# Kernel tuning notes

Hardware: AMD Instinct MI355X
Metric: run time of the kernel (lower is better)

## Reference

```python
import jax, jax.numpy as jnp
import numpy as np

B, L, T, LM, DFF, D, H = 8, 256, 2048, 4096, 1024, 84, 4
HD = D // H  # 21
NCLS = 265


def _ln(x, s, b):
    m = x.mean(-1, keepdims=True)
    v = ((x - m) ** 2).mean(-1, keepdims=True)
    return (x - m) * jax.lax.rsqrt(v + 1e-5) * s + b


def _fourier(xyz, gB):
    # PositionEmbeddingCoordsSine(d_pos=10, pos_type='fourier'): xyz @ B * 2pi -> [sin, cos]
    proj = (2.0 * jnp.pi) * jnp.einsum('bnc,cd->bnd', xyz, gB)  # [B,N,5]
    return jnp.concatenate([jnp.sin(proj), jnp.cos(proj)], axis=-1)  # [B,N,10]


def setup_inputs() -> dict:
    key = jax.random.key(0)
    ks = jax.random.split(key, 20)
    def nrm(k, shape, scale):
        return jax.random.normal(k, shape, jnp.float32) * scale
    coords = jax.random.uniform(ks[0], (B, L, 6), jnp.float32)
    cls = jax.random.randint(ks[1], (B, L), 0, NCLS).astype(jnp.float32)
    vision_features = jnp.concatenate([coords, cls[..., None]], axis=-1)  # [B,L,7]
    FIN = D * L + LM  # 25600
    inp = {
        'grd_tokens': nrm(ks[2], (T, LM), 1.0),
        'vision_features': vision_features,
        'token_batch_idx': jax.random.randint(ks[3], (T,), 0, B),
        'gauss_B': nrm(ks[4], (3, 5), 1.0),
        'class_emb': nrm(ks[5], (NCLS, 64), 0.02),
        'w_in': nrm(ks[6], (2, D, 3 * D), D ** -0.5),
        'b_in': jnp.zeros((2, 3 * D), jnp.float32),
        'w_out': nrm(ks[7], (2, D, D), D ** -0.5),
        'b_out': jnp.zeros((2, D), jnp.float32),
        'ln1_s': jnp.ones((2, D), jnp.float32), 'ln1_b': jnp.zeros((2, D), jnp.float32),
        'w_ff1': nrm(ks[8], (2, D, DFF), D ** -0.5), 'b_ff1': jnp.zeros((2, DFF), jnp.float32),
        'w_ff2': nrm(ks[9], (2, DFF, D), DFF ** -0.5), 'b_ff2': jnp.zeros((2, D), jnp.float32),
        'ln2_s': jnp.ones((2, D), jnp.float32), 'ln2_b': jnp.zeros((2, D), jnp.float32),
        'w0': nrm(ks[10], (FIN, DFF), FIN ** -0.5), 'b0': jnp.zeros((DFF,), jnp.float32),
        'w1': nrm(ks[11], (DFF, DFF), DFF ** -0.5), 'b1': jnp.zeros((DFF,), jnp.float32),
        'w2': nrm(ks[12], (DFF, DFF), DFF ** -0.5), 'b2': jnp.zeros((DFF,), jnp.float32),
        'w3': nrm(ks[13], (DFF, DFF), DFF ** -0.5), 'b3': jnp.zeros((DFF,), jnp.float32),
        'w4': nrm(ks[14], (DFF, 6), DFF ** -0.5), 'b4': jnp.zeros((6,), jnp.float32),
    }
    return inp


def reference(grd_tokens, vision_features, token_batch_idx, gauss_B, class_emb,
              w_in, b_in, w_out, b_out, ln1_s, ln1_b, w_ff1, b_ff1, w_ff2, b_ff2,
              ln2_s, ln2_b, w0, b0, w1, b1, w2, b2, w3, b3, w4, b4):
    pe_min = _fourier(vision_features[:, :, 0:3], gauss_B)  # [B,L,10]
    pe_max = _fourier(vision_features[:, :, 3:6], gauss_B)  # [B,L,10]
    cls = vision_features[:, :, -1].astype(jnp.int32)
    src = jnp.concatenate([pe_min, pe_max, class_emb[cls]], axis=-1)  # [B,L,84]
    pad = jnp.all(vision_features == 0, axis=-1)  # [B,L]
    neg = jnp.where(pad, -1e9, 0.0)[:, None, None, :]  # [B,1,1,L] key-padding bias
    # 2-layer post-norm transformer encoder (DETR-style, pos=None, dropout=0)
    for l in range(2):
        qkv = src @ w_in[l] + b_in[l]
        q, k, v = jnp.split(qkv, 3, axis=-1)
        q = q.reshape(B, L, H, HD)
        k = k.reshape(B, L, H, HD)
        v = v.reshape(B, L, H, HD)
        scores = jnp.einsum('blhd,bmhd->bhlm', q, k) / jnp.sqrt(jnp.float32(HD)) + neg
        attn = jax.nn.softmax(scores, axis=-1)
        o = jnp.einsum('bhlm,bmhd->blhd', attn, v).reshape(B, L, D)
        src = _ln(src + o @ w_out[l] + b_out[l], ln1_s[l], ln1_b[l])
        ff = jax.nn.relu(src @ w_ff1[l] + b_ff1[l]) @ w_ff2[l] + b_ff2[l]
        src = _ln(src + ff, ln2_s[l], ln2_b[l])
    vision_flat = src.reshape(B, L * D)  # flattened encoder output per sample [B, 21504]
    # batched version of the ragged python loop: gather per-token vision feat + concat lm feat
    feat = jnp.concatenate([vision_flat[token_batch_idx], grd_tokens], axis=-1)  # [T, 25600]
    h = jax.nn.relu(feat @ w0 + b0)
    h = jax.nn.relu(h @ w1 + b1)
    h = jax.nn.relu(h @ w2 + b2)
    h = jax.nn.relu(h @ w3 + b3)
    return h @ w4 + b4  # [T, 6]
```

## Files before the change

kernel.cpp:

```cpp
#include <hip/hip_runtime.h>
#include <hip/hip_bf16.h>

#define B_ 8
#define L_ 256
#define T_ 2048
#define LM_ 4096
#define DFF_ 1024
#define D_ 84
#define H_ 4
#define HD_ 21
#define BL_ (B_*L_)
#define VISF_ (L_*D_)
#define VKS 168
#define VCHUNK (VISF_/VKS)
#define AKS 8
#define AKEYS (L_/AKS)

typedef __attribute__((ext_vector_type(8))) short bf16x8;
typedef __attribute__((ext_vector_type(4))) float f32x4;

typedef const __attribute__((address_space(1))) int* gas_p;
typedef __attribute__((address_space(3))) int* las_p;
__device__ __forceinline__ void gld_lds16(const void* g, void* l) {
    __builtin_amdgcn_global_load_lds((gas_p)g, (las_p)l, 16, 0, 0);
}

__global__ void k_build_src(const float* __restrict__ vf, const float* __restrict__ gB,
                            const float* __restrict__ cemb, float* __restrict__ src,
                            float* __restrict__ neg)
{
    int row = blockIdx.x * blockDim.x + threadIdx.x;
    if (row >= BL_) return;
    float v[7];
    bool allz = true;
    #pragma unroll
    for (int c = 0; c < 7; ++c) { v[c] = vf[row*7 + c]; allz = allz && (v[c] == 0.0f); }
    neg[row] = allz ? -1e9f : 0.0f;
    float* s = src + (size_t)row * D_;
    const float TWO_PI = 6.28318530717958647692f;
    #pragma unroll
    for (int d = 0; d < 5; ++d) {
        float pmin = TWO_PI * (v[0]*gB[d] + v[1]*gB[5+d] + v[2]*gB[10+d]);
        float pmax = TWO_PI * (v[3]*gB[d] + v[4]*gB[5+d] + v[5]*gB[10+d]);
        s[d]      = sinf(pmin);  s[5+d]  = cosf(pmin);
        s[10+d]   = sinf(pmax);  s[15+d] = cosf(pmax);
    }
    int cls = (int)v[6];
    const float4* ce = reinterpret_cast<const float4*>(cemb + (size_t)cls*64);
    float4* so = reinterpret_cast<float4*>(s + 20);
    #pragma unroll
    for (int i = 0; i < 16; ++i) so[i] = ce[i];
}

__global__ __launch_bounds__(256) void k_qkv8(const float* __restrict__ src,
        const float* __restrict__ w_in, const float* __restrict__ b_in,
        float* __restrict__ qkv, int lay)
{
    __shared__ float s8[8][D_];
    int r0 = blockIdx.x * 8, tid = threadIdx.x;
    for (int idx = tid; idx < 8*D_; idx += 256) {
        int r = idx / D_, d = idx - r*D_;
        s8[r][d] = src[(size_t)(r0+r)*D_ + d];
    }
    __syncthreads();
    if (tid < 3*D_) {
        const float* w = w_in + (size_t)lay*D_*3*D_ + tid;
        float acc[8] = {};
        for (int d = 0; d < D_; ++d) {
            float wv = w[(size_t)d*3*D_];
            #pragma unroll
            for (int r = 0; r < 8; ++r) acc[r] = fmaf(s8[r][d], wv, acc[r]);
        }
        float bv = b_in[lay*3*D_ + tid];
        #pragma unroll
        for (int r = 0; r < 8; ++r) qkv[(size_t)(r0+r)*(3*D_) + tid] = acc[r] + bv;
    }
}

__global__ __launch_bounds__(256) void k_attn_part(const float* __restrict__ qkv,
        const float* __restrict__ neg, float* __restrict__ part)
{
    __shared__ float ks_[AKEYS*HD_], vs_[AKEYS*HD_], ns[AKEYS];
    int bh = blockIdx.x;
    int b = bh >> 2, h = bh & 3;
    int sp = blockIdx.y;
    int tid = threadIdx.x;
    int k0 = sp * AKEYS;
    for (int idx = tid; idx < AKEYS*HD_; idx += 256) {
        int l = idx / HD_, d = idx - l*HD_;
        size_t base = ((size_t)(b*L_ + k0 + l))*(3*D_) + h*HD_ + d;
        ks_[idx] = qkv[base + D_];
        vs_[idx] = qkv[base + 2*D_];
    }
    if (tid < AKEYS) ns[tid] = neg[b*L_ + k0 + tid];
    __syncthreads();
    float q[HD_];
    {
        size_t base = ((size_t)(b*L_ + tid))*(3*D_) + h*HD_;
        #pragma unroll
        for (int d = 0; d < HD_; ++d) q[d] = qkv[base + d];
    }
    const float scale = 0.21821789023599239f;
    float m_run = -INFINITY, l_run = 0.0f;
    float o[HD_];
    #pragma unroll
    for (int d = 0; d < HD_; ++d) o[d] = 0.0f;
    for (int m = 0; m < AKEYS; ++m) {
        const float* krow = &ks_[m*HD_];
        float sdot = 0.0f;
        #pragma unroll
        for (int d = 0; d < HD_; ++d) sdot = fmaf(q[d], krow[d], sdot);
        float sc = sdot * scale + ns[m];
        float nm = fmaxf(m_run, sc);
        float c = __expf(m_run - nm);
        float p = __expf(sc - nm);
        l_run = l_run * c + p;
        const float* vrow = &vs_[m*HD_];
        #pragma unroll
        for (int d = 0; d < HD_; ++d) o[d] = fmaf(p, vrow[d], o[d]*c);
        m_run = nm;
    }
    float* po = part + (((size_t)bh*AKS + sp)*L_ + tid)*24;
    #pragma unroll
    for (int d = 0; d < HD_; ++d) po[d] = o[d];
    po[21] = m_run;
    po[22] = l_run;
}

__global__ __launch_bounds__(64) void k_attn_merge(const float* __restrict__ part,
        float* __restrict__ attn_o)
{
    int bh = blockIdx.x;
    int b = bh >> 2, h = bh & 3;
    int q = blockIdx.y*64 + threadIdx.x;
    const float* pb = part + ((size_t)bh*AKS*L_ + q)*24;
    float m_tot = -INFINITY;
    #pragma unroll
    for (int sp = 0; sp < AKS; ++sp)
        m_tot = fmaxf(m_tot, pb[(size_t)sp*L_*24 + 21]);
    float l_tot = 0.0f;
    float o[HD_];
    #pragma unroll
    for (int d = 0; d < HD_; ++d) o[d] = 0.0f;
    #pragma unroll
    for (int sp = 0; sp < AKS; ++sp) {
        const float* pp = pb + (size_t)sp*L_*24;
        float e = __expf(pp[21] - m_tot);
        l_tot = fmaf(pp[22], e, l_tot);
        #pragma unroll
        for (int d = 0; d < HD_; ++d) o[d] = fmaf(pp[d], e, o[d]);
    }
    float inv = 1.0f / l_tot;
    float* op = attn_o + ((size_t)(b*L_ + q))*D_ + h*HD_;
    #pragma unroll
    for (int d = 0; d < HD_; ++d) op[d] = o[d]*inv;
}

__global__ __launch_bounds__(128) void k_oproj_ln(const float* __restrict__ attn_o,
        const float* __restrict__ w_out, const float* __restrict__ b_out,
        const float* __restrict__ ln_s, const float* __restrict__ ln_b,
        float* __restrict__ src, __hip_bfloat16* __restrict__ srcb, int lay)
{
    __shared__ float os[D_];
    __shared__ float r1[128], r2[128];
    int row = blockIdx.x, tid = threadIdx.x;
    if (tid < D_) os[tid] = attn_o[(size_t)row*D_ + tid];
    __syncthreads();
    float y = 0.0f;
    if (tid < D_) {
        const float* w = w_out + (size_t)lay*D_*D_ + tid;
        float acc = b_out[lay*D_ + tid];
        for (int d = 0; d < D_; ++d) acc = fmaf(os[d], w[(size_t)d*D_], acc);
        y = src[(size_t)row*D_ + tid] + acc;
    }
    r1[tid] = (tid < D_) ? y : 0.0f;
    r2[tid] = (tid < D_) ? y*y : 0.0f;
    __syncthreads();
    for (int s = 64; s > 0; s >>= 1) {
        if (tid < s) { r1[tid] += r1[tid+s]; r2[tid] += r2[tid+s]; }
        __syncthreads();
    }
    float mean = r1[0] * (1.0f/D_);
    float var  = r2[0] * (1.0f/D_) - mean*mean;
    float rstd = rsqrtf(var + 1e-5f);
    float out = 0.0f;
    if (tid < D_) {
        out = (y - mean)*rstd*ln_s[lay*D_+tid] + ln_b[lay*D_+tid];
        src[(size_t)row*D_ + tid] = out;
    }
    srcb[(size_t)row*128 + tid] = (tid < D_) ? __float2bfloat16(out)
                                             : __float2bfloat16(0.0f);
}

__global__ __launch_bounds__(256) void k_ff2_mfma(
        const __hip_bfloat16* __restrict__ hb,
        const __hip_bfloat16* __restrict__ wt,
        float* __restrict__ part)
{
    __shared__ __align__(16) __hip_bfloat16 sA[2][4096];
    __shared__ __align__(16) __hip_bfloat16 sB[2][6144];
    int tid = threadIdx.x;
    int bm = blockIdx.x * 64, sp = blockIdx.y;
    int wave = tid >> 6, lane = tid & 63;
    int wr = wave >> 1, wc = wave & 1;
    int l15 = lane & 15, l4 = lane >> 4;
    f32x4 acc[2][3] = {};

    const int a_m0 = tid & 63;
    const int b_i0 = tid,       b_kb0 = b_i0/96, b_n0 = b_i0%96;
    const int b_i1 = tid + 256, b_kb1 = b_i1/96, b_n1 = b_i1%96;
    const int b_i2 = tid + 512, b_kb2 = b_i2/96, b_n2 = b_i2%96;
    const __hip_bfloat16* Ap0 = hb + (size_t)(bm + a_m0)*1024 + sp*128 + (tid>>6)*8;
    const __hip_bfloat16* Ap1 = Ap0 + 32;
    const __hip_bfloat16* Bp0 = wt + (size_t)b_n0*1024 + sp*128 + b_kb0*8;
    const __hip_bfloat16* Bp1 = wt + (size_t)b_n1*1024 + sp*128 + b_kb1*8;
    const __hip_bfloat16* Bp2 = wt + (size_t)b_n2*1024 + sp*128 + b_kb2*8;

    gld_lds16(Ap0, (char*)&sA[0][0] + tid*16);
    gld_lds16(Ap1, (char*)&sA[0][0] + (tid+256)*16);
    gld_lds16(Bp0, (char*)&sB[0][0] + b_i0*16);
    gld_lds16(Bp1, (char*)&sB[0][0] + b_i1*16);
    gld_lds16(Bp2, (char*)&sB[0][0] + b_i2*16);
    #pragma unroll
    for (int t = 0; t < 2; ++t) {
        __syncthreads();
        if (t == 0) {
            gld_lds16(Ap0 + 64, (char*)&sA[1][0] + tid*16);
            gld_lds16(Ap1 + 64, (char*)&sA[1][0] + (tid+256)*16);
            gld_lds16(Bp0 + 64, (char*)&sB[1][0] + b_i0*16);
            gld_lds16(Bp1 + 64, (char*)&sB[1][0] + b_i1*16);
            gld_lds16(Bp2 + 64, (char*)&sB[1][0] + b_i2*16);
        }
        const __hip_bfloat16* sa = &sA[t][0];
        const __hip_bfloat16* sb = &sB[t][0];
        #pragma unroll
        for (int ks = 0; ks < 2; ++ks) {
            bf16x8 af[2], bfr[3];
            #pragma unroll
            for (int mi = 0; mi < 2; ++mi)
                af[mi] = *reinterpret_cast<const bf16x8*>(
                    &sa[(size_t)((ks*4 + l4)*64 + wr*32 + mi*16 + l15) * 8]);
            #pragma unroll
            for (int ni = 0; ni < 3; ++ni)
                bfr[ni] = *reinterpret_cast<const bf16x8*>(
                    &sb[(size_t)((ks*4 + l4)*96 + wc*48 + ni*16 + l15) * 8]);
            #pragma unroll
            for (int mi = 0; mi < 2; ++mi)
                #pragma unroll
                for (int ni = 0; ni < 3; ++ni)
                    acc[mi][ni] = __builtin_amdgcn_mfma_f32_16x16x32_bf16(
                        af[mi], bfr[ni], acc[mi][ni], 0, 0, 0);
        }
    }
    float* po = part + (size_t)sp*(2048*96);
    #pragma unroll
    for (int mi = 0; mi < 2; ++mi)
        #pragma unroll
        for (int reg = 0; reg < 4; ++reg) {
            int row = bm + wr*32 + mi*16 + l4*4 + reg;
            #pragma unroll
            for (int ni = 0; ni < 3; ++ni) {
                int col = wc*48 + ni*16 + l15;
                po[(size_t)row*96 + col] = acc[mi][ni][reg];
            }
        }
}

__global__ __launch_bounds__(128) void k_ff2ln_red(const float* __restrict__ part,
        const float* __restrict__ b_ff2, const float* __restrict__ ln_s,
        const float* __restrict__ ln_b, float* __restrict__ src, int lay)
{
    __shared__ float r1[128], r2[128];
    int row = blockIdx.x, tid = threadIdx.x;
    float y = 0.0f;
    if (tid < D_) {
        #pragma unroll
        for (int sp = 0; sp < 8; ++sp)
            y += part[(size_t)sp*(2048*96) + (size_t)row*96 + tid];
        y += b_ff2[lay*D_ + tid] + src[(size_t)row*D_ + tid];
    }
    r1[tid] = (tid < D_) ? y : 0.0f;
    r2[tid] = (tid < D_) ? y*y : 0.0f;
    __syncthreads();
    for (int s = 64; s > 0; s >>= 1) {
        if (tid < s) { r1[tid] += r1[tid+s]; r2[tid] += r2[tid+s]; }
        __syncthreads();
    }
    float mean = r1[0] * (1.0f/D_);
    float var  = r2[0] * (1.0f/D_) - mean*mean;
    float rstd = rsqrtf(var + 1e-5f);
    if (tid < D_)
        src[(size_t)row*D_ + tid] = (y - mean)*rstd*ln_s[lay*D_+tid] + ln_b[lay*D_+tid];
}

__global__ __launch_bounds__(256) void k_vis_gemm(const float* __restrict__ src,
        const float* __restrict__ w0, float* __restrict__ partials)
{
    __shared__ float vf[8][VCHUNK];
    __shared__ float red[8][256][4];
    int nt = blockIdx.x, sp = blockIdx.y, tid = threadIdx.x;
    int k0 = sp * VCHUNK;
    for (int idx = tid; idx < 8*VCHUNK; idx += 256) {
        int r = idx >> 7, c = idx & 127;
        vf[r][c] = src[(size_t)r*VISF_ + k0 + c];
    }
    __syncthreads();
    int ng = tid & 31;
    int kh = tid >> 5;
    const float* wp = w0 + (size_t)(k0 + kh*16)*DFF_ + nt*128 + ng*4;
    float acc[8][4] = {};
    #pragma unroll 4
    for (int kk = 0; kk < 16; ++kk) {
        float4 w = *reinterpret_cast<const float4*>(wp + (size_t)kk*DFF_);
        #pragma unroll
        for (int m = 0; m < 8; ++m) {
            float sv = vf[m][kh*16 + kk];
            acc[m][0] = fmaf(sv, w.x, acc[m][0]);
            acc[m][1] = fmaf(sv, w.y, acc[m][1]);
            acc[m][2] = fmaf(sv, w.z, acc[m][2]);
            acc[m][3] = fmaf(sv, w.w, acc[m][3]);
        }
    }
    #pragma unroll
    for (int m = 0; m < 8; ++m)
        *reinterpret_cast<float4*>(&red[m][tid][0]) =
            make_float4(acc[m][0], acc[m][1], acc[m][2], acc[m][3]);
    __syncthreads();
    int m2 = tid >> 5, ng2 = tid & 31;
    float4 s = *reinterpret_cast<const float4*>(&red[m2][ng2][0]);
    #pragma unroll
    for (int j = 1; j < 8; ++j) {
        float4 v = *reinterpret_cast<const float4*>(&red[m2][j*32 + ng2][0]);
        s.x += v.x; s.y += v.y; s.z += v.z; s.w += v.w;
    }
    *reinterpret_cast<float4*>(
        &partials[(size_t)sp*8192 + m2*1024 + nt*128 + ng2*4]) = s;
}

__global__ __launch_bounds__(256) void k_vis_red1(const float* __restrict__ partials,
        float* __restrict__ p2)
{
    int o = blockIdx.x*256 + threadIdx.x;
    int g = blockIdx.y;
    float s = 0.0f;
    #pragma unroll
    for (int j = 0; j < 14; ++j) s += partials[(size_t)(g*14 + j)*8192 + o];
    p2[(size_t)g*8192 + o] = s;
}

__global__ __launch_bounds__(256) void k_vis_red2(const float* __restrict__ p2,
        float* __restrict__ vis)
{
    int o = blockIdx.x*256 + threadIdx.x;
    float s = 0.0f;
    #pragma unroll
    for (int g = 0; g < 12; ++g) s += p2[(size_t)g*8192 + o];
    vis[o] = s;
}

struct bh4 { __hip_bfloat16 x, y, z, w; };

__global__ __launch_bounds__(256) void k_f2b(const float* __restrict__ in,
        __hip_bfloat16* __restrict__ out, int n4)
{
    int i = blockIdx.x*256 + threadIdx.x;
    if (i >= n4) return;
    float4 v = reinterpret_cast<const float4*>(in)[i];
    bh4 o = { __float2bfloat16(v.x), __float2bfloat16(v.y),
              __float2bfloat16(v.z), __float2bfloat16(v.w) };
    reinterpret_cast<bh4*>(out)[i] = o;
}

__global__ __launch_bounds__(256) void k_wT(const float* __restrict__ W,
        __hip_bfloat16* __restrict__ WT, int K, int N)
{
    __shared__ float t[32][33];
    int kb = blockIdx.x*32, nb = blockIdx.y*32;
    int tx = threadIdx.x & 31, ty = threadIdx.x >> 5;
    #pragma unroll
    for (int i = 0; i < 4; ++i)
        t[ty + i*8][tx] = W[(size_t)(kb + ty + i*8)*N + nb + tx];
    __syncthreads();
    #pragma unroll
    for (int i = 0; i < 4; ++i)
        WT[(size_t)(nb + ty + i*8)*K + kb + tx] = __float2bfloat16(t[tx][ty + i*8]);
}

__global__ __launch_bounds__(256) void k_wTp(const float* __restrict__ W,
        __hip_bfloat16* __restrict__ WT, int K, int N, int KP)
{
    __shared__ float t[32][33];
    int kb = blockIdx.x*32, nb = blockIdx.y*32;
    int tx = threadIdx.x & 31, ty = threadIdx.x >> 5;
    #pragma unroll
    for (int i = 0; i < 4; ++i) {
        int k = kb + ty + i*8, n = nb + tx;
        t[ty + i*8][tx] = (k < K && n < N) ? W[(size_t)k*N + n] : 0.0f;
    }
    __syncthreads();
    #pragma unroll
    for (int i = 0; i < 4; ++i)
        WT[(size_t)(nb + ty + i*8)*KP + kb + tx] = __float2bfloat16(t[tx][ty + i*8]);
}

template<bool ADD_VIS>
__global__ __launch_bounds__(256) void mfma_gemm(
        const __hip_bfloat16* __restrict__ A,
        const __hip_bfloat16* __restrict__ WT,
        const float* __restrict__ bias,
        const float* __restrict__ vis,
        const int* __restrict__ bidx,
        __hip_bfloat16* __restrict__ C,
        int K)
{
    constexpr int N = 1024;
    __shared__ __align__(16) __hip_bfloat16 sA[3][4096];
    __shared__ __align__(16) __hip_bfloat16 sB[3][4096];
    int tid = threadIdx.x;
    int bm = blockIdx.x * 64, bn = blockIdx.y * 64;
    int wave = tid >> 6, lane = tid & 63;
    int wr = wave >> 1, wc = wave & 1;
    int l15 = lane & 15, l4 = lane >> 4;
    f32x4 acc[2][2] = {};

    const __hip_bfloat16* Ap = A  + (size_t)(bm + (tid & 63))*K + (tid >> 6)*8;
    const __hip_bfloat16* Bp = WT + (size_t)(bn + (tid & 63))*K + (tid >> 6)*8;

    int nsteps = K >> 6;
    auto STAGE = [&](int t, int b) {
        int ko = t << 6;
        char* la = (char*)&sA[b][0];
        char* lb = (char*)&sB[b][0];
        gld_lds16(Ap + ko,      la + tid*16);
        gld_lds16(Ap + ko + 32, la + (tid+256)*16);
        gld_lds16(Bp + ko,      lb + tid*16);
        gld_lds16(Bp + ko + 32, lb + (tid+256)*16);
    };
    STAGE(0, 0);
    if (nsteps > 1) STAGE(1, 1);

    for (int t = 0; t < nsteps; ++t) {
        if (t + 2 < nsteps) {
            STAGE(t + 2, (t + 2) % 3);
            asm volatile("s_waitcnt vmcnt(8)" ::: "memory");
        } else if (t + 1 < nsteps) {
            asm volatile("s_waitcnt vmcnt(4)" ::: "memory");
        } else {
            asm volatile("s_waitcnt vmcnt(0)" ::: "memory");
        }
        __builtin_amdgcn_s_barrier();
        const __hip_bfloat16* sa = &sA[t % 3][0];
        const __hip_bfloat16* sb = &sB[t % 3][0];
        #pragma unroll
        for (int ks = 0; ks < 2; ++ks) {
            bf16x8 af[2], bfr[2];
            #pragma unroll
            for (int mi = 0; mi < 2; ++mi)
                af[mi] = *reinterpret_cast<const bf16x8*>(
                    &sa[(size_t)((ks*4 + l4)*64 + wr*32 + mi*16 + l15) * 8]);
            #pragma unroll
            for (int ni = 0; ni < 2; ++ni)
                bfr[ni] = *reinterpret_cast<const bf16x8*>(
                    &sb[(size_t)((ks*4 + l4)*64 + wc*32 + ni*16 + l15) * 8]);
            #pragma unroll
            for (int mi = 0; mi < 2; ++mi)
                #pragma unroll
                for (int ni = 0; ni < 2; ++ni)
                    acc[mi][ni] = __builtin_amdgcn_mfma_f32_16x16x32_bf16(
                        af[mi], bfr[ni], acc[mi][ni], 0, 0, 0);
        }
        __builtin_amdgcn_s_barrier();
    }

    #pragma unroll
    for (int mi = 0; mi < 2; ++mi) {
        #pragma unroll
        for (int reg = 0; reg < 4; ++reg) {
            int row = bm + wr*32 + mi*16 + l4*4 + reg;
            const float* vrow = nullptr;
            if (ADD_VIS) vrow = vis + (size_t)bidx[row]*1024;
            #pragma unroll
            for (int ni = 0; ni < 2; ++ni) {
                int col = bn + wc*32 + ni*16 + l15;
                float v = acc[mi][ni][reg] + bias[col];
                if (ADD_VIS) v += vrow[col];
                v = fmaxf(v, 0.0f);
                C[(size_t)row*N + col] = __float2bfloat16(v);
            }
        }
    }
}

__global__ __launch_bounds__(64) void k_final(const __hip_bfloat16* __restrict__ h,
        const float* __restrict__ w4, const float* __restrict__ b4, float* __restrict__ out)
{
    int t = blockIdx.x, lane = threadIdx.x;
    float acc[6] = {};
    for (int k = lane; k < DFF_; k += 64) {
        float hv = __bfloat162float(h[(size_t)t*DFF_ + k]);
        #pragma unroll
        for (int j = 0; j < 6; ++j) acc[j] = fmaf(hv, w4[k*6 + j], acc[j]);
    }
    #pragma unroll
    for (int j = 0; j < 6; ++j)
        #pragma unroll
        for (int s = 32; s > 0; s >>= 1) acc[j] += __shfl_down(acc[j], s);
    if (lane == 0) {
        #pragma unroll
        for (int j = 0; j < 6; ++j) out[(size_t)t*6 + j] = acc[j] + b4[j];
    }
}

extern "C" void kernel_launch(void* const* d_in, const int* in_sizes, int n_in,
                              void* d_out, int out_size, void* d_ws, size_t ws_size,
                              hipStream_t stream)
{
    const float* grd   = (const float*)d_in[0];
    const float* vfeat = (const float*)d_in[1];
    const int*   tbi   = (const int*)  d_in[2];
    const float* gB    = (const float*)d_in[3];
    const float* cemb  = (const float*)d_in[4];
    const float* w_in  = (const float*)d_in[5];
    const float* b_in  = (const float*)d_in[6];
    const float* w_out = (const float*)d_in[7];
    const float* b_out = (const float*)d_in[8];
    const float* ln1_s = (const float*)d_in[9];
    const float* ln1_b = (const float*)d_in[10];
    const float* w_ff1 = (const float*)d_in[11];
    const float* b_ff1 = (const float*)d_in[12];
    const float* w_ff2 = (const float*)d_in[13];
    const float* b_ff2 = (const float*)d_in[14];
    const float* ln2_s = (const float*)d_in[15];
    const float* ln2_b = (const float*)d_in[16];
    const float* w0    = (const float*)d_in[17];
    const float* b0    = (const float*)d_in[18];
    const float* w1    = (const float*)d_in[19];
    const float* b1    = (const float*)d_in[20];
    const float* w2    = (const float*)d_in[21];
    const float* b2    = (const float*)d_in[22];
    const float* w3    = (const float*)d_in[23];
    const float* b3    = (const float*)d_in[24];
    const float* w4    = (const float*)d_in[25];
    const float* b4    = (const float*)d_in[26];

    float* ws = (float*)d_ws;
    float* src    = ws;
    float* neg    = src    + 172032;
    float* qkv    = neg    + 2048;
    float* attn_o = qkv    + 516096;
    float* vparts = attn_o + 172032;
    float* vp2    = vparts + 1376256;
    float* visp   = vp2    + 98304;
    float* ffpart = visp   + 8192;
    float* fend   = ffpart + 1572864;
    __hip_bfloat16* grdb  = (__hip_bfloat16*)fend;
    __hip_bfloat16* w0t   = grdb  + 8388608;
    __hip_bfloat16* w1t   = w0t   + 4194304;
    __hip_bfloat16* w2t   = w1t   + 1048576;
    __hip_bfloat16* w3t   = w2t   + 1048576;
    __hip_bfloat16* hab   = w3t   + 1048576;
    __hip_bfloat16* hbb   = hab   + 2097152;
    __hip_bfloat16* srcb  = hbb   + 2097152;
    __hip_bfloat16* wff1t = srcb  + 262144;
    __hip_bfloat16* wff2t = wff1t + 262144;
    __hip_bfloat16* ffh   = hab;

    k_f2b<<<(T_*LM_/4 + 255)/256, 256, 0, stream>>>(grd, grdb, T_*LM_/4);
    k_wT<<<dim3(LM_/32,  DFF_/32), 256, 0, stream>>>(w0 + (size_t)VISF_*DFF_, w0t, LM_,  DFF_);
    k_wT<<<dim3(DFF_/32, DFF_/32), 256, 0, stream>>>(w1, w1t, DFF_, DFF_);
    k_wT<<<dim3(DFF_/32, DFF_/32), 256, 0, stream>>>(w2, w2t, DFF_, DFF_);
    k_wT<<<dim3(DFF_/32, DFF_/32), 256, 0, stream>>>(w3, w3t, DFF_, DFF_);
    for (int l = 0; l < 2; ++l) {
        k_wTp<<<dim3(128/32, 1024/32), 256, 0, stream>>>(
            w_ff1 + (size_t)l*D_*DFF_, wff1t + (size_t)l*1024*128, D_, DFF_, 128);
        k_wTp<<<dim3(1024/32, 96/32),  256, 0, stream>>>(
            w_ff2 + (size_t)l*DFF_*D_, wff2t + (size_t)l*96*1024, DFF_, D_, 1024);
    }

    k_build_src<<<8, 256, 0, stream>>>(vfeat, gB, cemb, src, neg);

    for (int lay = 0; lay < 2; ++lay) {
        k_qkv8      <<<BL_/8, 256, 0, stream>>>(src, w_in, b_in, qkv, lay);
        k_attn_part <<<dim3(B_*H_, AKS), 256, 0, stream>>>(qkv, neg, ffpart);
        k_attn_merge<<<dim3(B_*H_, 4), 64, 0, stream>>>(ffpart, attn_o);
        k_oproj_ln  <<<BL_, 128, 0, stream>>>(attn_o, w_out, b_out, ln1_s, ln1_b, src, srcb, lay);
        mfma_gemm<false><<<dim3(32, 16), 256, 0, stream>>>(
            srcb, wff1t + (size_t)lay*1024*128, b_ff1 + lay*DFF_,
            nullptr, nullptr, ffh, 128);
        k_ff2_mfma<<<dim3(32, 8), 256, 0, stream>>>(
            ffh, wff2t + (size_t)lay*96*1024, ffpart);
        k_ff2ln_red<<<BL_, 128, 0, stream>>>(ffpart, b_ff2, ln2_s, ln2_b, src, lay);
    }

    k_vis_gemm<<<dim3(8, VKS), 256, 0, stream>>>(src, w0, vparts);
    k_vis_red1<<<dim3(32, 12), 256, 0, stream>>>(vparts, vp2);
    k_vis_red2<<<32, 256, 0, stream>>>(vp2, visp);

    dim3 mg(T_/64, DFF_/64);
    mfma_gemm<true ><<<mg, 256, 0, stream>>>(grdb, w0t, b0, visp, tbi, hab, LM_);
    mfma_gemm<false><<<mg, 256, 0, stream>>>(hab,  w1t, b1, nullptr, nullptr, hbb, DFF_);
    mfma_gemm<false><<<mg, 256, 0, stream>>>(hbb,  w2t, b2, nullptr, nullptr, hab, DFF_);
    mfma_gemm<false><<<mg, 256, 0, stream>>>(hab,  w3t, b3, nullptr, nullptr, hbb, DFF_);

    k_final<<<T_, 64, 0, stream>>>(hbb, w4, b4, (float*)d_out);
}
```

Measured before the change: 290.3 us.

## Fuse attention merge into o-proj, single-pass vis reduction, 128-K double-buffered GEMM

Folds the attention split-merge into the output-projection/LayerNorm kernel, so each block merges its own row's partial softmax state and the separate merge launch plus its attn_o round trip are gone. The two-stage vision partial reduction becomes a single kernel that sums all 168 partials per output. The MFMA GEMM moves from triple-buffered 64-wide K steps to double-buffered 128-wide K steps, halving barriers per K at the cost of a shallower prefetch pipeline. The single-stage reduction runs only 32 blocks with a long serial loop, and the merge work inside o-proj is recomputed per head element.

```diff
diff --git a/kernel.cpp b/kernel.cpp
--- a/kernel.cpp
+++ b/kernel.cpp
@@ -127,36 +127,7 @@
     po[22] = l_run;
 }
 
-__global__ __launch_bounds__(64) void k_attn_merge(const float* __restrict__ part,
-        float* __restrict__ attn_o)
-{
-    int bh = blockIdx.x;
-    int b = bh >> 2, h = bh & 3;
-    int q = blockIdx.y*64 + threadIdx.x;
-    const float* pb = part + ((size_t)bh*AKS*L_ + q)*24;
-    float m_tot = -INFINITY;
-    #pragma unroll
-    for (int sp = 0; sp < AKS; ++sp)
-        m_tot = fmaxf(m_tot, pb[(size_t)sp*L_*24 + 21]);
-    float l_tot = 0.0f;
-    float o[HD_];
-    #pragma unroll
-    for (int d = 0; d < HD_; ++d) o[d] = 0.0f;
-    #pragma unroll
-    for (int sp = 0; sp < AKS; ++sp) {
-        const float* pp = pb + (size_t)sp*L_*24;
-        float e = __expf(pp[21] - m_tot);
-        l_tot = fmaf(pp[22], e, l_tot);
-        #pragma unroll
-        for (int d = 0; d < HD_; ++d) o[d] = fmaf(pp[d], e, o[d]);
-    }
-    float inv = 1.0f / l_tot;
-    float* op = attn_o + ((size_t)(b*L_ + q))*D_ + h*HD_;
-    #pragma unroll
-    for (int d = 0; d < HD_; ++d) op[d] = o[d]*inv;
-}
-
-__global__ __launch_bounds__(128) void k_oproj_ln(const float* __restrict__ attn_o,
+__global__ __launch_bounds__(128) void k_oproj_ln(const float* __restrict__ part,
         const float* __restrict__ w_out, const float* __restrict__ b_out,
         const float* __restrict__ ln_s, const float* __restrict__ ln_b,
         float* __restrict__ src, __hip_bfloat16* __restrict__ srcb, int lay)
@@ -164,7 +135,24 @@
     __shared__ float os[D_];
     __shared__ float r1[128], r2[128];
     int row = blockIdx.x, tid = threadIdx.x;
-    if (tid < D_) os[tid] = attn_o[(size_t)row*D_ + tid];
+    int b = row >> 8, q = row & 255;
+    if (tid < D_) {
+        int h = tid / 21, d = tid - h*21;
+        const float* pb = part + (((size_t)(b*H_ + h)*AKS)*L_ + q)*24;
+        float m_tot = -INFINITY;
+        #pragma unroll
+        for (int sp = 0; sp < AKS; ++sp)
+            m_tot = fmaxf(m_tot, pb[(size_t)sp*L_*24 + 21]);
+        float l_tot = 0.0f, ov = 0.0f;
+        #pragma unroll
+        for (int sp = 0; sp < AKS; ++sp) {
+            const float* pp = pb + (size_t)sp*L_*24;
+            float e = __expf(pp[21] - m_tot);
+            l_tot = fmaf(pp[22], e, l_tot);
+            ov = fmaf(pp[d], e, ov);
+        }
+        os[tid] = ov / l_tot;
+    }
     __syncthreads();
     float y = 0.0f;
     if (tid < D_) {
@@ -337,24 +325,12 @@
         &partials[(size_t)sp*8192 + m2*1024 + nt*128 + ng2*4]) = s;
 }
 
-__global__ __launch_bounds__(256) void k_vis_red1(const float* __restrict__ partials,
-        float* __restrict__ p2)
-{
-    int o = blockIdx.x*256 + threadIdx.x;
-    int g = blockIdx.y;
-    float s = 0.0f;
-    #pragma unroll
-    for (int j = 0; j < 14; ++j) s += partials[(size_t)(g*14 + j)*8192 + o];
-    p2[(size_t)g*8192 + o] = s;
-}
-
-__global__ __launch_bounds__(256) void k_vis_red2(const float* __restrict__ p2,
+__global__ __launch_bounds__(256) void k_vis_red(const float* __restrict__ partials,
         float* __restrict__ vis)
 {
     int o = blockIdx.x*256 + threadIdx.x;
     float s = 0.0f;
-    #pragma unroll
-    for (int g = 0; g < 12; ++g) s += p2[(size_t)g*8192 + o];
+    for (int sp = 0; sp < VKS; ++sp) s += partials[(size_t)sp*8192 + o];
     vis[o] = s;
 }
 
@@ -414,8 +390,8 @@
         int K)
 {
     constexpr int N = 1024;
-    __shared__ __align__(16) __hip_bfloat16 sA[3][4096];
-    __shared__ __align__(16) __hip_bfloat16 sB[3][4096];
+    __shared__ __align__(16) __hip_bfloat16 sA[2][8192];
+    __shared__ __align__(16) __hip_bfloat16 sB[2][8192];
     int tid = threadIdx.x;
     int bm = blockIdx.x * 64, bn = blockIdx.y * 64;
     int wave = tid >> 6, lane = tid & 63;
@@ -426,33 +402,30 @@
     const __hip_bfloat16* Ap = A  + (size_t)(bm + (tid & 63))*K + (tid >> 6)*8;
     const __hip_bfloat16* Bp = WT + (size_t)(bn + (tid & 63))*K + (tid >> 6)*8;
 
-    int nsteps = K >> 6;
+    int nsteps = K >> 7;
     auto STAGE = [&](int t, int b) {
-        int ko = t << 6;
+        int ko = t << 7;
         char* la = (char*)&sA[b][0];
         char* lb = (char*)&sB[b][0];
-        gld_lds16(Ap + ko,      la + tid*16);
-        gld_lds16(Ap + ko + 32, la + (tid+256)*16);
-        gld_lds16(Bp + ko,      lb + tid*16);
-        gld_lds16(Bp + ko + 32, lb + (tid+256)*16);
+        #pragma unroll
+        for (int r = 0; r < 4; ++r) {
+            gld_lds16(Ap + ko + r*32, la + (tid + r*256)*16);
+            gld_lds16(Bp + ko + r*32, lb + (tid + r*256)*16);
+        }
     };
     STAGE(0, 0);
-    if (nsteps > 1) STAGE(1, 1);
-
     for (int t = 0; t < nsteps; ++t) {
-        if (t + 2 < nsteps) {
-            STAGE(t + 2, (t + 2) % 3);
+        if (t + 1 < nsteps) {
+            STAGE(t + 1, (t + 1) & 1);
             asm volatile("s_waitcnt vmcnt(8)" ::: "memory");
-        } else if (t + 1 < nsteps) {
-            asm volatile("s_waitcnt vmcnt(4)" ::: "memory");
         } else {
             asm volatile("s_waitcnt vmcnt(0)" ::: "memory");
         }
         __builtin_amdgcn_s_barrier();
-        const __hip_bfloat16* sa = &sA[t % 3][0];
-        const __hip_bfloat16* sb = &sB[t % 3][0];
-        #pragma unroll
-        for (int ks = 0; ks < 2; ++ks) {
+        const __hip_bfloat16* sa = &sA[t & 1][0];
+        const __hip_bfloat16* sb = &sB[t & 1][0];
+        #pragma unroll
+        for (int ks = 0; ks < 4; ++ks) {
             bf16x8 af[2], bfr[2];
             #pragma unroll
             for (int mi = 0; mi < 2; ++mi)
@@ -582,8 +555,7 @@
     for (int lay = 0; lay < 2; ++lay) {
         k_qkv8      <<<BL_/8, 256, 0, stream>>>(src, w_in, b_in, qkv, lay);
         k_attn_part <<<dim3(B_*H_, AKS), 256, 0, stream>>>(qkv, neg, ffpart);
-        k_attn_merge<<<dim3(B_*H_, 4), 64, 0, stream>>>(ffpart, attn_o);
-        k_oproj_ln  <<<BL_, 128, 0, stream>>>(attn_o, w_out, b_out, ln1_s, ln1_b, src, srcb, lay);
+        k_oproj_ln  <<<BL_, 128, 0, stream>>>(ffpart, w_out, b_out, ln1_s, ln1_b, src, srcb, lay);
         mfma_gemm<false><<<dim3(32, 16), 256, 0, stream>>>(
             srcb, wff1t + (size_t)lay*1024*128, b_ff1 + lay*DFF_,
             nullptr, nullptr, ffh, 128);
@@ -593,8 +565,7 @@
     }
 
     k_vis_gemm<<<dim3(8, VKS), 256, 0, stream>>>(src, w0, vparts);
-    k_vis_red1<<<dim3(32, 12), 256, 0, stream>>>(vparts, vp2);
-    k_vis_red2<<<32, 256, 0, stream>>>(vp2, visp);
+    k_vis_red<<<32, 256, 0, stream>>>(vparts, visp);
 
     dim3 mg(T_/64, DFF_/64);
     mfma_gemm<true ><<<mg, 256, 0, stream>>>(grdb, w0t, b0, visp, tbi, hab, LM_);
```

Measured after the change: 294.6 us. Within noise of the previous version (+1.5%).
